# Optimization experiments

Hardware: AMD Instinct MI355X
Metric: run time of the kernel (lower is better)

## Reference

```python
import jax, jax.numpy as jnp
import numpy as np

# (pt, eta, phi) feature indices per particle for each block (eta=None for MET)
A_PT, A_ETA, A_PHI = [5, 4, 35, 34], [9, 8, 45, 44], [13, 12, 55, 54]            # e3,e2,j9,j8
B_PT, B_ETA, B_PHI = [3, 33, 31, 2], [7, 43, 41, 6], [11, 53, 51, 10]            # e1,j7,j5,e0
C_PT, C_ETA, C_PHI = [28, 32, 15, 16], [38, 42, 19, 20], [48, 52, 23, 24]        # j2,j6,mu1,mu2
D_PT, D_ETA, D_PHI = [0, 14, 30, 26, 29, 27, 17], [None, 18, 40, 36, 39, 37, 21], [1, 22, 50, 46, 49, 47, 25]  # MET,mu0,j4,j0,j3,j1,mu3


def _bc(a, nd):
    # broadcast a (B,) or () angle factor over nd trailing qubit axes
    return a.reshape(a.shape + (1,) * nd)


def _rx(state, theta, w):
    nd = state.ndim - 2
    c = _bc(jnp.cos(theta * 0.5), nd)
    s = _bc(jnp.sin(theta * 0.5), nd)
    s0 = jnp.take(state, 0, axis=w + 1)
    s1 = jnp.take(state, 1, axis=w + 1)
    return jnp.stack([c * s0 - 1j * s * s1, -1j * s * s0 + c * s1], axis=w + 1)


def _ry(state, theta, w):
    nd = state.ndim - 2
    c = _bc(jnp.cos(theta * 0.5), nd)
    s = _bc(jnp.sin(theta * 0.5), nd)
    s0 = jnp.take(state, 0, axis=w + 1)
    s1 = jnp.take(state, 1, axis=w + 1)
    return jnp.stack([c * s0 - s * s1, s * s0 + c * s1], axis=w + 1)


def _rz(state, theta, w):
    nd = state.ndim - 2
    ph = _bc(jnp.exp(-0.5j * theta.astype(state.dtype)), nd)
    s0 = jnp.take(state, 0, axis=w + 1)
    s1 = jnp.take(state, 1, axis=w + 1)
    return jnp.stack([ph * s0, jnp.conj(ph) * s1], axis=w + 1)


def _cnot(state, ctrl, tgt):
    c0 = jnp.take(state, 0, axis=ctrl + 1)
    c1 = jnp.take(state, 1, axis=ctrl + 1)
    t_ax = tgt + 1 if tgt < ctrl else tgt  # ctrl axis removed shifts higher wires down
    c1 = jnp.flip(c1, axis=t_ax)
    return jnp.stack([c0, c1], axis=ctrl + 1)


def _extract(x, pt_idx, eta_idx, phi_idx):
    pt = x[:, np.array(pt_idx)]
    eta = jnp.stack([x[:, i] if i is not None else jnp.zeros(x.shape[0], x.dtype) for i in eta_idx], axis=1)
    phi = x[:, np.array(phi_idx)]
    return pt, eta, phi


def _run_block(pt, eta, phi, weights, n, latent, trash, depth):
    B = pt.shape[0]
    state = jnp.zeros((B,) + (2,) * n, dtype=jnp.complex64)
    state = state.at[(slice(None),) + (0,) * n].set(1.0)
    for k in range(n):
        state = _rx(state, eta[:, k], k)
        state = _ry(state, pt[:, k], k)
        state = _rz(state, phi[:, k], k)
    for k in range(n - 1):
        state = _cnot(state, k, k + 1)
    for k in range(n):
        state = _rz(state, eta[:, k], k)
        state = _ry(state, pt[:, k], k)
        state = _rx(state, phi[:, k], k)
    for d in range(depth):
        for t in trash:
            for l in latent:
                state = _cnot(state, t, l)
        for k in range(n):
            state = _ry(state, weights[d * n + k], k)
        for l in latent:
            for t in trash:
                state = _cnot(state, l, t)
    p = jnp.abs(state) ** 2  # (B, 2,...,2) real probabilities
    red = tuple(range(1, n))
    zs = [jnp.sum(jnp.take(p, 0, axis=w + 1), axis=red) - jnp.sum(jnp.take(p, 1, axis=w + 1), axis=red) for w in trash]
    return jnp.stack(zs, axis=1)


def setup_inputs() -> dict:
    key = jax.random.key(0)
    k0, k1, k2, k3, k4 = jax.random.split(key, 5)
    B = 131072
    x = jax.random.normal(k0, (B, 56), dtype=jnp.float32)
    wA = 0.01 * jax.random.normal(k1, (4,), dtype=jnp.float32)
    wB = 0.01 * jax.random.normal(k2, (4,), dtype=jnp.float32)
    wC = 0.01 * jax.random.normal(k3, (4,), dtype=jnp.float32)
    wD = 0.01 * jax.random.normal(k4, (28,), dtype=jnp.float32)
    return {"x": x, "wA": wA, "wB": wB, "wC": wC, "wD": wD}


def reference(x, wA, wB, wC, wD):
    zA = _run_block(*_extract(x, A_PT, A_ETA, A_PHI), wA, 4, (0, 1), (2, 3), 1)  # (B,2)
    zB = _run_block(*_extract(x, B_PT, B_ETA, B_PHI), wB, 4, (0, 1), (2, 3), 1)  # (B,2)
    zC = _run_block(*_extract(x, C_PT, C_ETA, C_PHI), wC, 4, (0, 1), (2, 3), 1)  # (B,2)
    zD = _run_block(*_extract(x, D_PT, D_ETA, D_PHI), wD, 7, (0, 1, 2, 3), (4, 5, 6), 4)  # (B,3)
    return jnp.concatenate([zA, zB, zC, zD], axis=1)  # (B,9) ~ dict values concatenated
```

## Files before the change

### kernel.cpp

```cpp
#include <hip/hip_runtime.h>
#include <hip/hip_fp16.h>


#define DEVINL __device__ __forceinline__

typedef _Float16 hv2 __attribute__((ext_vector_type(2)));
typedef unsigned int u32;
typedef u32 vreg16 __attribute__((ext_vector_type(16)));
typedef u32 vreg64 __attribute__((ext_vector_type(64)));

struct C2 { __half2 rr, mp; };

DEVINL C2 mkc(float re, float im) {
  C2 c; c.rr = __floats2half2_rn(re, re); c.mp = __floats2half2_rn(-im, im); return c;
}
DEVINL __half2 mkamp(float re, float im) { return __floats2half2_rn(re, im); }
DEVINL __half2 swap2(__half2 v) { return __lowhigh2highlow(v); }
DEVINL __half2 cmulc(C2 u, __half2 v) { return __hfma2(u.rr, v, __hmul2(u.mp, swap2(v))); }

DEVINL float ampsq(__half2 v, float acc) {
#if __has_builtin(__builtin_amdgcn_fdot2)
  return __builtin_amdgcn_fdot2(__builtin_bit_cast(hv2, v), __builtin_bit_cast(hv2, v), acc, false);
#else
  float2 f = __half22float2(v);
  return fmaf(f.x, f.x, fmaf(f.y, f.y, acc));
#endif
}

constexpr int parc(int x) { x ^= x >> 4; x ^= x >> 2; x ^= x >> 1; return x & 1; }

struct c32 { float x, y; };
DEVINL c32 cmulf(c32 a, c32 b) { return { a.x*b.x - a.y*b.y, a.x*b.y + a.y*b.x }; }

template<class VT>
DEVINL __half2 vget(const VT& A, int i) { return __builtin_bit_cast(__half2, (u32)A[i]); }
template<class VT>
DEVINL void vset(VT& A, int i, __half2 v) { A[i] = __builtin_bit_cast(u32, v); }

DEVINL __half2 lx1(__half2 v) {
  int q = __shfl_xor(__builtin_bit_cast(int, v), 1, 64);
  return __builtin_bit_cast(__half2, q);
}
DEVINL float lx1f(float v) { return __shfl_xor(v, 1, 64); }


template<int N, int W, class VT>
DEVINL void g_ry(VT& A, __half2 c2, __half2 s2, __half2 ns2) {
  constexpr int M = 1 << (N - 1 - W);
#pragma unroll
  for (int i = 0; i < (1 << N); ++i) if (!(i & M)) {
    const int j = i | M;
    __half2 v0 = vget(A, i), v1 = vget(A, j);
    vset(A, i, __hfma2(c2, v0, __hmul2(ns2, v1)));
    vset(A, j, __hfma2(c2, v1, __hmul2(s2, v0)));
  }
}

template<int N, int W, class VT>
DEVINL void g_u2(VT& A, C2 u00, C2 u01, C2 u10, C2 u11) {
  constexpr int M = 1 << (N - 1 - W);
#pragma unroll
  for (int i = 0; i < (1 << N); ++i) if (!(i & M)) {
    const int j = i | M;
    __half2 v0 = vget(A, i), v1 = vget(A, j), v0s = swap2(v0), v1s = swap2(v1);
    vset(A, i, __hfma2(u00.rr, v0, __hfma2(u00.mp, v0s, __hfma2(u01.rr, v1, __hmul2(u01.mp, v1s)))));
    vset(A, j, __hfma2(u10.rr, v0, __hfma2(u10.mp, v0s, __hfma2(u11.rr, v1, __hmul2(u11.mp, v1s)))));
  }
}

template<int N, int C, int T, class VT>
DEVINL void g_cnot(VT& A) {
  constexpr int CM = 1 << (N - 1 - C), TM = 1 << (N - 1 - T);
#pragma unroll
  for (int i = 0; i < (1 << N); ++i) if ((i & CM) && !(i & TM)) {
    const int j = i | TM;
    __half2 t = vget(A, i); vset(A, i, vget(A, j)); vset(A, j, t);
  }
}

template<int N, int K, class VT>
DEVINL void chain_cnot(VT& A) {
  if constexpr (K < N - 1) { g_cnot<N, K, K + 1>(A); chain_cnot<N, K + 1>(A); }
}


DEVINL void mk_u01(float ce, float se, float cp, float sp, float cf, float sf,
                   c32& u0, c32& u1) {
  u0 = cmulf({cf, -sf}, {cp * ce, sp * se});
  u1 = cmulf({cf,  sf}, {sp * ce, -cp * se});
}

DEVINL void mk_U(float ce, float se, float cp, float sp, float cf, float sf,
                 C2& U00, C2& U01, C2& U10, C2& U11) {
  c32 z = {ce, -se}, zb = {ce, se};
  c32 A = cmulf({cf * cp, -sf * sp}, z);
  c32 T = cmulf({cf * sp,  sf * cp}, zb);
  c32 Cc = cmulf({cf * sp, -sf * cp}, z);
  c32 D = cmulf({cf * cp,  sf * sp}, zb);
  U00 = mkc(A.x, A.y); U01 = mkc(-T.x, -T.y); U10 = mkc(Cc.x, Cc.y); U11 = mkc(D.x, D.y);
}

DEVINL void load_sc(const float* __restrict__ xr, int eta_i, int pt_i, int phi_i,
                    float& ce, float& se, float& cp, float& sp, float& cf, float& sf) {
  float e = (eta_i < 0) ? 0.f : xr[eta_i];
  __sincosf(0.5f * e, &se, &ce);
  __sincosf(0.5f * xr[pt_i], &sp, &cp);
  __sincosf(0.5f * xr[phi_i], &sf, &cf);
}

template<int N, int M, class VT, class CF>
DEVINL void build_rec(VT& A, CF cf) {
  if constexpr (M < N) {
    c32 u0, u1; cf(M, u0, u1);
    C2 c0 = mkc(u0.x, u0.y), c1 = mkc(u1.x, u1.y);
#pragma unroll
    for (int j = (1 << M) - 1; j >= 0; --j) {
      __half2 s = vget(A, j);
      vset(A, 2 * j,     cmulc(c0, s));
      vset(A, 2 * j + 1, cmulc(c1, s));
    }
    build_rec<N, M + 1>(A, cf);
  }
}

template<int N, int K, class VT, class CF>
DEVINL void usweep_rec(VT& A, CF cf) {
  if constexpr (K < N) {
    C2 U00, U01, U10, U11;
    cf(K, U00, U01, U10, U11);
    g_u2<N, K>(A, U00, U01, U10, U11);
    usweep_rec<N, K + 1>(A, cf);
  }
}

template<int N, int K, class VT, class CF>
DEVINL void ry_rec(VT& A, CF cf) {
  if constexpr (K < N) {
    __half2 c2, s2, ns2;
    cf(K, c2, s2, ns2);
    g_ry<N, K>(A, c2, s2, ns2);
    ry_rec<N, K + 1>(A, cf);
  }
}


template<int I>
DEVINL void sim4h(const float* __restrict__ xr, const float* __restrict__ w, float* z) {
  constexpr int PT[3][4]  = {{5, 4, 35, 34}, {3, 33, 31, 2}, {28, 32, 15, 16}};
  constexpr int ETA[3][4] = {{9, 8, 45, 44}, {7, 43, 41, 6}, {38, 42, 19, 20}};
  constexpr int PHI[3][4] = {{13, 12, 55, 54}, {11, 53, 51, 10}, {48, 52, 23, 24}};
  vreg16 A;
  vset(A, 0, mkamp(1.f, 0.f));
  build_rec<4, 0>(A, [&](int M, c32& u0, c32& u1) {
    float ce, se, cp, sp, cf, sf;
    load_sc(xr, ETA[I][M], PT[I][M], PHI[I][M], ce, se, cp, sp, cf, sf);
    mk_u01(ce, se, cp, sp, cf, sf, u0, u1);
  });
  chain_cnot<4, 0>(A);
  usweep_rec<4, 0>(A, [&](int K, C2& U00, C2& U01, C2& U10, C2& U11) {
    float ce, se, cp, sp, cf, sf;
    load_sc(xr, ETA[I][K], PT[I][K], PHI[I][K], ce, se, cp, sp, cf, sf);
    mk_U(ce, se, cp, sp, cf, sf, U00, U01, U10, U11);
  });

#pragma unroll
  for (int i = 0; i < 16; ++i)
    if (parc(i & 3) && !(i & 8)) {
      __half2 t = vget(A, i); vset(A, i, vget(A, i ^ 12)); vset(A, i ^ 12, t);
    }

  ry_rec<4, 0>(A, [&](int K, __half2& c2, __half2& s2, __half2& ns2) {
    float sv, cv; __sincosf(0.5f * w[K], &sv, &cv);
    c2 = __floats2half2_rn(cv, cv);
    s2 = __floats2half2_rn(sv, sv);
    ns2 = __floats2half2_rn(-sv, -sv);
  });

#pragma unroll
  for (int i = 0; i < 16; ++i)
    if (parc(i & 12) && !(i & 2)) {
      __half2 t = vget(A, i); vset(A, i, vget(A, i ^ 3)); vset(A, i ^ 3, t);
    }

  float cls[4];
#pragma unroll
  for (int c = 0; c < 4; ++c) cls[c] = 0.f;
#pragma unroll
  for (int i = 0; i < 16; ++i) cls[i & 3] = ampsq(vget(A, i), cls[i & 3]);
  float z0 = 0.f, z1 = 0.f;
#pragma unroll
  for (int c = 0; c < 4; ++c) {
    z0 += (c & 2) ? -cls[c] : cls[c];
    z1 += (c & 1) ? -cls[c] : cls[c];
  }
  z[0] = z0; z[1] = z1;
}


DEVINL void role7(const float* __restrict__ xr, const float* __restrict__ wD,
                  float* __restrict__ out_row, bool po) {
  constexpr int PT[7]  = {0, 14, 30, 26, 29, 27, 17};
  constexpr int ETA[7] = {-1, 18, 40, 36, 39, 37, 21};
  constexpr int PHI[7] = {1, 22, 50, 46, 49, 47, 25};

  vreg64 A;
  vset(A, 0, mkamp(1.f, 0.f));
  build_rec<6, 0>(A, [&](int M, c32& u0, c32& u1) {
    const int k = M + 1;
    float ce, se, cp, sp, cf, sf;
    load_sc(xr, ETA[k], PT[k], PHI[k], ce, se, cp, sp, cf, sf);
    mk_u01(ce, se, cp, sp, cf, sf, u0, u1);
  });
  {
    float ce, se, cp, sp, cf, sf;
    load_sc(xr, ETA[0], PT[0], PHI[0], ce, se, cp, sp, cf, sf);
    c32 u0, u1; mk_u01(ce, se, cp, sp, cf, sf, u0, u1);
    C2 c0 = mkc(po ? u1.x : u0.x, po ? u1.y : u0.y);
#pragma unroll
    for (int i = 0; i < 64; ++i) vset(A, i, cmulc(c0, vget(A, i)));
  }

#pragma unroll
  for (int i = 0; i < 32; ++i) {
    const int j = i | 32;
    __half2 lo = vget(A, i), hi = vget(A, j);
    vset(A, i, po ? hi : lo);
    vset(A, j, po ? lo : hi);
  }
  chain_cnot<6, 0>(A);

  {
    float ce, se, cp, sp, cf, sf;
    load_sc(xr, ETA[0], PT[0], PHI[0], ce, se, cp, sp, cf, sf);
    C2 U00, U01, U10, U11;
    mk_U(ce, se, cp, sp, cf, sf, U00, U01, U10, U11);
    C2 UA, UB;
    UA.rr = po ? U11.rr : U00.rr; UA.mp = po ? U11.mp : U00.mp;
    UB.rr = po ? U10.rr : U01.rr; UB.mp = po ? U10.mp : U01.mp;
#pragma unroll
    for (int i = 0; i < 64; ++i) {
      __half2 m = vget(A, i), q = lx1(m);
      vset(A, i, __hfma2(UA.rr, m, __hfma2(UA.mp, swap2(m),
                 __hfma2(UB.rr, q, __hmul2(UB.mp, swap2(q))))));
    }
  }
  usweep_rec<6, 0>(A, [&](int W, C2& U00, C2& U01, C2& U10, C2& U11) {
    const int k = W + 1;
    float ce, se, cp, sp, cf, sf;
    load_sc(xr, ETA[k], PT[k], PHI[k], ce, se, cp, sp, cf, sf);
    mk_U(ce, se, cp, sp, cf, sf, U00, U01, U10, U11);
  });

#pragma unroll 1
  for (int d = 0; d < 4; ++d) {
#pragma unroll
    for (int i = 0; i < 64; ++i)
      if (parc(i & 7) && !(i & 0x20)) {
        const int j = i ^ 0x38;
        __half2 t0 = lx1(vget(A, j));
        __half2 t1 = lx1(vget(A, i));
        vset(A, i, t0); vset(A, j, t1);
      }

    {
      float sv, cv; __sincosf(0.5f * wD[7 * d], &sv, &cv);
      __half2 c2v = __floats2half2_rn(cv, cv);
      __half2 sp2 = __floats2half2_rn(po ? sv : -sv, po ? sv : -sv);
#pragma unroll
      for (int i = 0; i < 64; ++i) {
        __half2 q = lx1(vget(A, i));
        vset(A, i, __hfma2(c2v, vget(A, i), __hmul2(sp2, q)));
      }
    }
    ry_rec<6, 0>(A, [&](int W, __half2& c2, __half2& s2, __half2& ns2) {
      float sv, cv; __sincosf(0.5f * wD[7 * d + W + 1], &sv, &cv);
      c2 = __floats2half2_rn(cv, cv);
      s2 = __floats2half2_rn(sv, sv);
      ns2 = __floats2half2_rn(-sv, -sv);
    });

#pragma unroll
    for (int i = 0; i < 64; ++i)
      if (!(i & 4)) {
        const int j = i ^ 7;
        const bool cond = parc(i & 0x38) ? !po : po;
        __half2 lo = vget(A, i), hi = vget(A, j);
        vset(A, i, cond ? hi : lo);
        vset(A, j, cond ? lo : hi);
      }
  }

  float cls[8];
#pragma unroll
  for (int c = 0; c < 8; ++c) cls[c] = 0.f;
#pragma unroll
  for (int i = 0; i < 64; ++i) cls[i & 7] = ampsq(vget(A, i), cls[i & 7]);
  float z4 = 0.f, z5 = 0.f, z6 = 0.f;
#pragma unroll
  for (int c = 0; c < 8; ++c) {
    z4 += (c & 4) ? -cls[c] : cls[c];
    z5 += (c & 2) ? -cls[c] : cls[c];
    z6 += (c & 1) ? -cls[c] : cls[c];
  }
  z4 += lx1f(z4); z5 += lx1f(z5); z6 += lx1f(z6);
  if (!po) {
    out_row[6] = z4; out_row[7] = z5; out_row[8] = z6;
  }
}


__global__ void
__attribute__((amdgpu_flat_work_group_size(256, 256), amdgpu_waves_per_eu(2, 4)))
k_all(const float* __restrict__ x,
      const float* __restrict__ wA, const float* __restrict__ wB,
      const float* __restrict__ wC, const float* __restrict__ wD,
      float* __restrict__ out, int B) {
  const int base = blockIdx.x * 64;
  const int wv = threadIdx.x >> 6;
  const int lane = threadIdx.x & 63;

  if (wv == 0) {
    const int b = base + lane;
    if (b >= B) return;
    const float* xr = x + (size_t)b * 56;
    float o[4];
    sim4h<0>(xr, wA, &o[0]);
    sim4h<1>(xr, wB, &o[2]);
    float* op = out + (size_t)b * 9;
    op[0] = o[0]; op[1] = o[1]; op[2] = o[2]; op[3] = o[3];
  } else if (wv == 3) {
    const int b = base + lane;
    if (b >= B) return;
    const float* xr = x + (size_t)b * 56;
    float o[2];
    sim4h<2>(xr, wC, o);
    float* op = out + (size_t)b * 9;
    op[4] = o[0]; op[5] = o[1];
  } else {
    const int p = (wv - 1) * 32 + (lane >> 1);
    const int b = base + p;
    if (b >= B) return;
    const bool po = (lane & 1) != 0;
    role7(x + (size_t)b * 56, wD, out + (size_t)b * 9, po);
  }
}


extern "C" void kernel_launch(void* const* d_in, const int* in_sizes, int n_in,
                              void* d_out, int out_size, void* d_ws, size_t ws_size,
                              hipStream_t stream) {
  const float* x  = (const float*)d_in[0];
  const float* wA = (const float*)d_in[1];
  const float* wB = (const float*)d_in[2];
  const float* wC = (const float*)d_in[3];
  const float* wD = (const float*)d_in[4];
  float* out = (float*)d_out;
  const int B = in_sizes[0] / 56;

  const int blocks = (B + 63) / 64;
  k_all<<<blocks, 256, 0, stream>>>(x, wA, wB, wC, wD, out, B);
}
```

Measured before the change: 145.8 us.

## Split work into separate homogeneous blocks for small circuits and 7-qubit pairs

Before, each 256-thread block mixed roles: one wave ran blocks A and B, one ran C, and two waves ran the paired 7-qubit circuit, all for the same 64 rows. Now the grid is split: the first gx blocks give each thread one row and run A, B and C, and the remaining blocks run only the 7-qubit role with two threads per row. This removes the imbalance between waves with unequal work inside a block and makes each block uniform. It also changes the launch bounds to __launch_bounds__(256,2), which may alter register allocation and occupancy for the register-heavy 7-qubit path, and the two block types no longer share locality on x rows.

```diff
diff --git a/kernel.cpp b/kernel.cpp
--- a/kernel.cpp
+++ b/kernel.cpp
@@ -309,38 +309,28 @@
 }
 
 
-__global__ void
-__attribute__((amdgpu_flat_work_group_size(256, 256), amdgpu_waves_per_eu(2, 4)))
+__global__ void __launch_bounds__(256, 2)
 k_all(const float* __restrict__ x,
       const float* __restrict__ wA, const float* __restrict__ wB,
       const float* __restrict__ wC, const float* __restrict__ wD,
-      float* __restrict__ out, int B) {
-  const int base = blockIdx.x * 64;
-  const int wv = threadIdx.x >> 6;
-  const int lane = threadIdx.x & 63;
-
-  if (wv == 0) {
-    const int b = base + lane;
+      float* __restrict__ out, int B, int gx) {
+  const int bx = blockIdx.x;
+  if (bx < gx) {
+    const int b = bx * 256 + threadIdx.x;
     if (b >= B) return;
     const float* xr = x + (size_t)b * 56;
-    float o[4];
+    float o[6];
     sim4h<0>(xr, wA, &o[0]);
     sim4h<1>(xr, wB, &o[2]);
+    sim4h<2>(xr, wC, &o[4]);
     float* op = out + (size_t)b * 9;
-    op[0] = o[0]; op[1] = o[1]; op[2] = o[2]; op[3] = o[3];
-  } else if (wv == 3) {
-    const int b = base + lane;
+#pragma unroll
+    for (int i = 0; i < 6; ++i) op[i] = o[i];
+  } else {
+    const int t = (bx - gx) * 256 + threadIdx.x;
+    const int b = t >> 1;
     if (b >= B) return;
-    const float* xr = x + (size_t)b * 56;
-    float o[2];
-    sim4h<2>(xr, wC, o);
-    float* op = out + (size_t)b * 9;
-    op[4] = o[0]; op[5] = o[1];
-  } else {
-    const int p = (wv - 1) * 32 + (lane >> 1);
-    const int b = base + p;
-    if (b >= B) return;
-    const bool po = (lane & 1) != 0;
+    const bool po = (t & 1) != 0;
     role7(x + (size_t)b * 56, wD, out + (size_t)b * 9, po);
   }
 }
@@ -356,7 +346,9 @@
   const float* wD = (const float*)d_in[4];
   float* out = (float*)d_out;
   const int B = in_sizes[0] / 56;
-
-  const int blocks = (B + 63) / 64;
-  k_all<<<blocks, 256, 0, stream>>>(x, wA, wB, wC, wD, out, B);
-}
+  const int threads = 256;
+
+  const int gx = (B + threads - 1) / threads;
+  const int gy = (2 * B + threads - 1) / threads;
+  k_all<<<gx + gy, threads, 0, stream>>>(x, wA, wB, wC, wD, out, B, gx);
+}
```

New measurement: 138.4 us. 1.05x faster.
